# Optimization experiments

Hardware: AMD Instinct MI355X
Metric: run time of the kernel (lower is better)

## Reference

```python
import jax, jax.numpy as jnp
import numpy as np

N = 8192   # num_nodes
H = 128    # hidden_dim
B = 100    # batch of events
K = 5      # num_neg_samples
TD_MAX = 10000.0
TIME_SD = jnp.array([50.0, 7.0, 15.0, 15.0])  # time_sd from forward; time_mean = 0


def setup_inputs() -> dict:
    key = jax.random.key(0)
    ks = jax.random.split(key, 16)
    p = 32.0 / N  # avg degree ~32
    A = (jax.random.uniform(ks[0], (N, N)) < p).astype(jnp.float32)
    # S init: S[v,u] = 1/D[v] for neighbors u (row-normalized A)
    S = A / (A.sum(axis=1, keepdims=True) + 1e-7)
    z0 = jax.random.normal(ks[1], (N, H)) * 0.1
    u = jax.random.randint(ks[2], (B,), 0, N)
    v = jax.random.randint(ks[3], (B,), 0, N)
    event_types = jax.random.randint(ks[4], (B,), 0, 2)
    neg_idx = jax.random.randint(ks[5], (B, 2 * K), 0, N)
    time_diff = jax.random.normal(ks[6], (B, 2, 4))
    t_bar = jax.random.uniform(ks[7], (B, N)) * 1000.0
    t = 1000.0 + 10.0 * jnp.arange(B, dtype=jnp.float32)

    def lin(k, o, i):
        k1, k2 = jax.random.split(k)
        lim = 1.0 / np.sqrt(i)
        return (jax.random.uniform(k1, (o, i), minval=-lim, maxval=lim),
                jax.random.uniform(k2, (o,), minval=-lim, maxval=lim))

    om0_w, om0_b = lin(ks[8], 1, 2 * H)
    om1_w, om1_b = lin(ks[9], 1, 2 * H)
    Wh_w, Wh_b = lin(ks[10], H, H)
    Ws_w, Ws_b = lin(ks[11], H, H)
    Wr_w, Wr_b = lin(ks[12], H, H)
    Wt_w, Wt_b = lin(ks[13], H, 4)
    return dict(u=u, v=v, event_types=event_types, neg_idx=neg_idx,
                time_diff=time_diff, t_bar=t_bar, t=t, z0=z0, A=A, S=S,
                w_t=0.5 * jnp.ones(2), alpha=0.5 * jnp.ones(2), psi=0.5 * jnp.ones(2),
                om0_w=om0_w, om0_b=om0_b, om1_w=om1_w, om1_b=om1_b,
                Wh_w=Wh_w, Wh_b=Wh_b, Ws_w=Ws_w, Ws_b=Ws_b,
                Wr_w=Wr_w, Wr_b=Wr_b, Wt_w=Wt_w, Wt_b=Wt_b)


def _forward(u, v, event_types, neg_idx, time_diff, t_bar, t, z0, A, S,
             w_t, alpha, psi, om0_w, om0_b, om1_w, om1_b,
             Wh_w, Wh_b, Ws_w, Ws_b, Wr_w, Wr_b, Wt_w, Wt_b):
    td_norm = time_diff / TIME_SD  # (td - 0) / sd

    def hawkes(zu, zv, et, td):
        # lambda = psi * log(1 + exp(g/psi)) + alpha * exp(-w_t * td/td_max)
        zc = jnp.concatenate([zu, zv], axis=-1)
        g0 = jnp.einsum('...d,d->...', zc, om0_w[0]) + om0_b[0]
        g1 = jnp.einsum('...d,d->...', zc, om1_w[0]) + om1_b[0]
        g = jnp.where(et == 0, g0, g1)
        ps, al, wt = psi[et], alpha[et], w_t[et]
        gp = jnp.clip(g / (ps + 1e-7), -75.0, 75.0)
        return ps * jnp.log1p(jnp.exp(gp)) + al * jnp.exp(-wt * (td / TD_MAX))

    ar = jnp.arange(N)

    def step(z, ev):
        u_it, v_it, et, td2, tb, t_it, neg = ev
        z_u, z_v = z[u_it], z[v_it]
        Wh_all = z @ Wh_w.T + Wh_b  # [N,H]

        def struct(node):
            # structural attention over node's neighbors (masked, not dense loop)
            mask = A[node] > 0
            q = jnp.exp(S[node]) * mask
            q = q / (q.sum() + 1e-7)
            hsig = jax.nn.sigmoid(q[:, None] * Wh_all)
            hmax = jnp.where(mask[:, None], hsig, -jnp.inf).max(axis=0)
            return jnp.where(jnp.any(mask), hmax, 0.0)

        # update of u uses struct info from v's neighborhood, and vice versa
        hs = jnp.stack([struct(v_it), struct(u_it)])  # [2,H]
        h = (hs @ Ws_w.T + Ws_b) + (jnp.stack([z_u, z_v]) @ Wr_w.T + Wr_b) + (td2 @ Wt_w.T + Wt_b)
        z_upd = jax.nn.sigmoid(h)
        z_new = z.at[u_it].set(z_upd[0]).at[v_it].set(z_upd[1])

        # negative pairs: (u, v_neg_k) then (u_neg_k, v), using z_prev
        v_neg, u_neg = neg[:K], neg[K:]
        zu_neg = jnp.concatenate([jnp.broadcast_to(z_u, (K, H)), z[u_neg]], 0)
        zv_neg = jnp.concatenate([z[v_neg], jnp.broadcast_to(z_v, (K, H))], 0)
        lt_u = jnp.concatenate([jnp.full((K,), tb[u_it]), tb[u_neg]])
        lt_v = jnp.concatenate([tb[v_neg], jnp.full((K,), tb[v_it])])
        ts_neg = t_it - jnp.maximum(lt_u, lt_v)
        ts_pos = t_it - jnp.maximum(tb[u_it], tb[v_it])

        # all-node intensity prediction (Lambda_dict path, detached in torch)
        zd = jax.lax.stop_gradient(z)
        zu_all = jnp.concatenate([jnp.broadcast_to(jax.lax.stop_gradient(z_u), (N, H)),
                                  jnp.broadcast_to(jax.lax.stop_gradient(z_v), (N, H))], 0)
        zv_all = jnp.concatenate([zd, zd], 0)
        last_t = jnp.maximum(
            jnp.concatenate([jnp.full((N,), tb[u_it]), jnp.full((N,), tb[v_it])]),
            jnp.concatenate([tb, tb]))
        lam_all = hawkes(zu_all, zv_all, jnp.full((2 * N,), et),
                         jax.lax.stop_gradient(t_it - last_t))
        m = ((ar != u_it) & (ar != v_it)).astype(lam_all.dtype)
        lam_sum = jax.lax.stop_gradient(jnp.sum(lam_all * jnp.concatenate([m, m])))

        return z_new, (z_u, z_v, zu_neg, zv_neg, ts_pos, ts_neg, lam_sum)

    _, (zu_p, zv_p, zun, zvn, ts_p, ts_n, lam_sums) = jax.lax.scan(
        step, z0, (u, v, event_types, td_norm, t_bar, t, neg_idx))

    lam_pos = hawkes(zu_p, zv_p, event_types, ts_p)            # [B]
    lam_neg = hawkes(zun, zvn, event_types[:, None], ts_n)      # [B,2K]
    return jnp.concatenate([lam_pos[:, None], lam_neg, lam_sums[:, None]], axis=1)  # [B, 2K+2]


def reference(u, v, event_types, neg_idx, time_diff, t_bar, t, z0, A, S,
              w_t, alpha, psi, om0_w, om0_b, om1_w, om1_b,
              Wh_w, Wh_b, Ws_w, Ws_b, Wr_w, Wr_b, Wt_w, Wt_b):
    return _forward(u, v, event_types, neg_idx, time_diff, t_bar, t, z0, A, S,
                    w_t, alpha, psi, om0_w, om0_b, om1_w, om1_b,
                    Wh_w, Wh_b, Ws_w, Ws_b, Wr_w, Wr_b, Wt_w, Wt_b)
```

## Files before the change

### kernel.cpp

```cpp
#include <hip/hip_runtime.h>
#include <math.h>

#define N 8192
#define H 128
#define BB 100
#define KK 5
#define MAXN 256
#define TD_MAXF 10000.0f

#define OFF_WHALLV ((size_t)N * H)
#define OFF_ZVER (OFF_WHALLV + 2 * BB * H)
#define WH_LDW 132

#define AGENT_LD(p) \
  __hip_atomic_load((p), __ATOMIC_RELAXED, __HIP_MEMORY_SCOPE_AGENT)
#define AGENT_ST(p, v) \
  __hip_atomic_store((p), (v), __ATOMIC_RELAXED, __HIP_MEMORY_SCOPE_AGENT)

__global__ __launch_bounds__(256) void prep2_kernel(
    const float* __restrict__ z0, const float* __restrict__ om0,
    const float* __restrict__ om1, float* __restrict__ dvec0,
    unsigned* __restrict__ done) {
  if (blockIdx.x == 32) {
    if (threadIdx.x < 4) AGENT_ST(&done[threadIdx.x], 0u);
    return;
  }
  int j = blockIdx.x * 256 + threadIdx.x;
  const float4* zr = (const float4*)(z0 + (size_t)j * H);
  const float4* o0 = (const float4*)om0;
  const float4* o1 = (const float4*)om1;
  float a0 = 0, b0 = 0, a1 = 0, b1 = 0;
  for (int k = 0; k < H / 4; ++k) {
    float4 zv = zr[k];
    float4 l0 = o0[k], r0 = o0[k + H / 4];
    float4 l1 = o1[k], r1 = o1[k + H / 4];
    a0 += zv.x * l0.x + zv.y * l0.y + zv.z * l0.z + zv.w * l0.w;
    b0 += zv.x * r0.x + zv.y * r0.y + zv.z * r0.z + zv.w * r0.w;
    a1 += zv.x * l1.x + zv.y * l1.y + zv.z * l1.z + zv.w * l1.w;
    b1 += zv.x * r1.x + zv.y * r1.y + zv.z * r1.z + zv.w * r1.w;
  }
  dvec0[0 * N + j] = a0;
  dvec0[1 * N + j] = b0;
  dvec0[2 * N + j] = a1;
  dvec0[3 * N + j] = b1;
}

__global__ __launch_bounds__(1024, 4) void fused_kernel(
    const int* __restrict__ u_, const int* __restrict__ v_,
    const int* __restrict__ et_, const int* __restrict__ neg_,
    const float* __restrict__ time_diff, const float* __restrict__ t_bar,
    const float* __restrict__ tt, const float* __restrict__ z0,
    const float* __restrict__ A, const float* __restrict__ S,
    const float* __restrict__ Wh, const float* __restrict__ Ws,
    const float* __restrict__ Wr, const float* __restrict__ Wh_b,
    const float* __restrict__ Ws_b, const float* __restrict__ Wr_b,
    const float* __restrict__ Wt_w, const float* __restrict__ Wt_b,
    const float* __restrict__ w_t, const float* __restrict__ alpha,
    const float* __restrict__ psi, const float* __restrict__ om0_w,
    const float* __restrict__ om1_w, const float* __restrict__ om0_b,
    const float* __restrict__ om1_b, const float* __restrict__ wsf,
    float* __restrict__ zver, float* __restrict__ whallv,
    float* __restrict__ dlog, const float* __restrict__ dvec0,
    unsigned* done, float* __restrict__ out) {
  const int blk = blockIdx.x;
  const int t = threadIdx.x;
  __shared__ __align__(16) float WhL[H * WH_LDW];
  __shared__ float scratch[8][2][H];
  __shared__ float hsS[2][H];
  __shared__ float zrowS[2][H];
  __shared__ float zupdS[2][H];
  __shared__ float td2S[2][4];
  __shared__ int nidxS[2][MAXN];
  __shared__ float nqS[2][MAXN];
  __shared__ int woffS[2][MAXN];
  __shared__ int cMS[2];
  __shared__ int zsrcS[2];
  __shared__ unsigned needS[4];
  __shared__ int uL[BB], vL[BB];
  __shared__ int wsumI[16];
  __shared__ float wsumF[16];
  __shared__ float dR[N];
  __shared__ float red[1024];
  __shared__ float suS, svS;

  if (blk < BB) {
    const int b = blk;
    const int r = t >> 9;
    const int tr = t & 511;
    const int sub = (t >> 7) & 3;
    const int d = t & (H - 1);
    const int ks = t >> 7;
    const int k0 = ks * 16;

    if (t < BB) {
      uL[t] = u_[t];
      vL[t] = v_[t];
    }
    if (t >= 512 && t < 520) {
      int i = t - 512;
      int cc = i & 3;
      float sd = (cc == 0) ? 50.0f : ((cc == 1) ? 7.0f : 15.0f);
      td2S[i >> 2][cc] = time_diff[b * 8 + i] / sd;
    }
    if (t >= 1020) needS[t - 1020] = 0u;
    {
      const float4* wh4 = (const float4*)Wh;
      float4* whl4 = (float4*)WhL;
      for (int i = t; i < H * H / 4; i += 1024)
        whl4[(i >> 5) * 33 + (i & 31)] = wh4[i];
    }
    const float whb = Wh_b[d];
    float wsReg[16], wrReg[16], whReg[16];
#pragma unroll
    for (int kk = 0; kk < 16; ++kk) {
      wsReg[kk] = Ws[(size_t)d * H + k0 + kk];
      wrReg[kk] = Wr[(size_t)d * H + k0 + kk];
      whReg[kk] = Wh[(size_t)d * H + k0 + kk];
    }
    float biasReg = 0.0f;
    float4 wt4Reg = {0.0f, 0.0f, 0.0f, 0.0f};
    if (t < 256) {
      int dd = t & (H - 1);
      biasReg = Ws_b[dd] + Wr_b[dd] + Wt_b[dd];
      wt4Reg = ((const float4*)Wt_w)[dd];
    }
    float omA = 0.0f, omB = 0.0f;
    if (t >= 256 && t < 768) {
      int w = (t - 256) >> 6;
      int lane6 = t & 63;
      int which = w & 3;
      int wsel = which >> 1;
      int offo = (which & 1) * H;
      const float* omw = wsel ? om1_w : om0_w;
      omA = omw[offo + lane6];
      omB = omw[offo + 64 + lane6];
    }

    const int node = r ? u_[b] : v_[b];
    unsigned hm = 0u;
    int c = 0;
    float local = 0.0f;
    for (int it = 0; it < N / 512; ++it) {
      int j = it * 512 + tr;
      if (A[(size_t)node * N + j] > 0.0f) {
        hm |= 1u << it;
        ++c;
        local += expf(S[(size_t)node * N + j]);
      }
    }
    const int lane = t & 63;
    const int wv = t >> 6;
    int ex = c;
    for (int s2 = 1; s2 < 64; s2 <<= 1) {
      int o = __shfl_up(ex, s2);
      if (lane >= s2) ex += o;
    }
    float ls = local;
    for (int s2 = 32; s2 > 0; s2 >>= 1) ls += __shfl_down(ls, s2);
    if (lane == 63) wsumI[wv] = ex;
    if (lane == 0) wsumF[wv] = ls;
    ex -= c;
    __syncthreads();

    int base0 = 0, ctot = 0;
    float qs = 0.0f;
    {
      int w0 = r * 8;
#pragma unroll
      for (int w = 0; w < 8; ++w) {
        int wi = w0 + w;
        int cw = wsumI[wi];
        if (wi < wv) base0 += cw;
        ctot += cw;
        qs += wsumF[wi];
      }
    }
    const float iq = 1.0f / (qs + 1e-7f);
    int p = base0 + ex;
    for (int it = 0; it < N / 512; ++it) {
      if ((hm >> it) & 1u) {
        int j = it * 512 + tr;
        if (p < MAXN) {
          nidxS[r][p] = j;
          nqS[r][p] = expf(S[(size_t)node * N + j]);
        }
        ++p;
      }
    }
    const int cM = min(ctot, MAXN);
    if (tr == 0) cMS[r] = cM;
    __syncthreads();

    for (int i = tr; i < cM; i += 512) {
      int n = nidxS[r][i];
      int a = -1, row = 0;
      for (int s2 = b - 1; s2 >= 0; --s2) {
        if (vL[s2] == n) { a = s2; row = 1; break; }
        if (uL[s2] == n) { a = s2; row = 0; break; }
      }
      woffS[r][i] = (a < 0) ? n * H : (int)OFF_WHALLV + (2 * a + row) * H;
      nqS[r][i] *= iq;
      if (a >= 0) atomicOr(&needS[a >> 5], 1u << (a & 31));
    }
    if (t < 2) {
      int nd = t ? vL[b] : uL[b];
      int a = -1, row = 0;
      for (int s2 = b - 1; s2 >= 0; --s2) {
        if (vL[s2] == nd) { a = s2; row = 1; break; }
        if (uL[s2] == nd) { a = s2; row = 0; break; }
      }
      zsrcS[t] = (a >= 0) ? 2 * a + row : -1;
      if (a >= 0) atomicOr(&needS[a >> 5], 1u << (a & 31));
    }
    __syncthreads();

    float zpre = 0.0f;
    int zs = -1;
    if (t < 256) {
      int rr = t >> 7, dd = t & (H - 1);
      zs = zsrcS[rr];
      if (zs < 0) {
        int nd = rr ? vL[b] : uL[b];
        zpre = z0[(size_t)nd * H + dd];
      }
    }

    float mx = -INFINITY;
    {
      const float4* WhL4 = (const float4*)WhL;
      for (int i = sub; i < cM; i += 4) {
        int off = woffS[r][i];
        if (off < (int)OFF_WHALLV) {
          const float4* zr4 = (const float4*)(z0 + (size_t)(off >> 7) * H);
          float acc = whb;
#pragma unroll 8
          for (int m = 0; m < 32; ++m) {
            float4 zv = zr4[m];
            float4 wvv = WhL4[d * 33 + m];
            acc += zv.x * wvv.x + zv.y * wvv.y + zv.z * wvv.z + zv.w * wvv.w;
          }
          mx = fmaxf(mx, nqS[r][i] * acc);
        }
      }
    }
    if (t == 0) {
      for (int w = 0; w < 4; ++w) {
        unsigned nw = needS[w];
        if (!nw) continue;
        while ((AGENT_LD(&done[w]) & nw) != nw) __builtin_amdgcn_s_sleep(1);
      }
    }
    __syncthreads();

    const int ub = uL[b], vb = vL[b];

    for (int i = sub; i < cM; i += 4) {
      int off = woffS[r][i];
      if (off >= (int)OFF_WHALLV)
        mx = fmaxf(mx, nqS[r][i] * AGENT_LD(&wsf[(size_t)off + d]));
    }
    scratch[sub][r][d] = mx;
    if (t < 256) {
      int rr = t >> 7, dd = t & (H - 1);
      zrowS[rr][dd] =
          (zs < 0) ? zpre : AGENT_LD(&wsf[OFF_ZVER + (size_t)zs * H + dd]);
    }
    __syncthreads();

    if (t < 2 * H) {
      int rr = t >> 7, dd = t & (H - 1);
      float m = fmaxf(fmaxf(scratch[0][rr][dd], scratch[1][rr][dd]),
                      fmaxf(scratch[2][rr][dd], scratch[3][rr][dd]));
      hsS[rr][dd] = (cMS[rr] > 0) ? (1.0f / (1.0f + expf(-m))) : 0.0f;
    }
    __syncthreads();

    {
      float a0 = 0.0f, a1 = 0.0f;
#pragma unroll
      for (int kk = 0; kk < 16; ++kk) {
        int k = k0 + kk;
        a0 += hsS[0][k] * wsReg[kk] + zrowS[0][k] * wrReg[kk];
        a1 += hsS[1][k] * wsReg[kk] + zrowS[1][k] * wrReg[kk];
      }
      scratch[ks][0][d] = a0;
      scratch[ks][1][d] = a1;
    }
    __syncthreads();

    if (t < 2 * H) {
      int rr = t >> 7, dd = t & (H - 1);
      float acc = biasReg;
#pragma unroll
      for (int kx = 0; kx < 8; ++kx) acc += scratch[kx][rr][dd];
      acc += td2S[rr][0] * wt4Reg.x + td2S[rr][1] * wt4Reg.y +
             td2S[rr][2] * wt4Reg.z + td2S[rr][3] * wt4Reg.w;
      float zu = 1.0f / (1.0f + expf(-acc));
      zupdS[rr][dd] = zu;
      AGENT_ST(&zver[(size_t)(2 * b + rr) * H + dd], zu);
    }
    __syncthreads();

    {
      int r0 = (ub == vb) ? 1 : 0;
      float f0 = 0.0f, f1 = 0.0f;
#pragma unroll
      for (int kk = 0; kk < 16; ++kk) {
        int k = k0 + kk;
        f0 += zupdS[r0][k] * whReg[kk];
        f1 += zupdS[1][k] * whReg[kk];
      }
      scratch[ks][0][d] = f0;
      scratch[ks][1][d] = f1;
    }
    __syncthreads();

    if (t < 2 * H) {
      int rr = t >> 7, dd = t & (H - 1);
      float acc = whb;
#pragma unroll
      for (int kx = 0; kx < 8; ++kx) acc += scratch[kx][rr][dd];
      AGENT_ST(&whallv[(size_t)(2 * b + rr) * H + dd], acc);
    } else if (t < 768) {
      int w = (t - 256) >> 6;
      int lane6 = t & 63;
      int row = w >> 2;
      int which = w & 3;
      int rr = (row == 0 && ub == vb) ? 1 : row;
      float val = zupdS[rr][lane6] * omA + zupdS[rr][64 + lane6] * omB;
      for (int s2 = 32; s2 > 0; s2 >>= 1) val += __shfl_down(val, s2);
      if (lane6 == 0) AGENT_ST(&dlog[b * 8 + which * 2 + row], val);
    }
    __syncthreads();

    if (t == 0) {
      asm volatile("s_waitcnt vmcnt(0)" ::: "memory");
      __hip_atomic_fetch_or(&done[b >> 5], 1u << (b & 31), __ATOMIC_RELAXED,
                            __HIP_MEMORY_SCOPE_AGENT);
    }
    return;
  }

  const int b = blk - BB;
  const int e = et_[b];
  const int ub = u_[b], vb = v_[b];
  const float ps = psi[e], al = alpha[e], wt = w_t[e];
  const float ob0 = om0_b[0], ob1 = om1_b[0];
  const float ob = e ? ob1 : ob0;
  const float tcur = tt[b];
  const float inv_ps = 1.0f / (ps + 1e-7f);
  const int whichR = 2 * e + 1;
  const int whichL = 2 * e;

  if (t < BB) {
    uL[t] = u_[t];
    vL[t] = v_[t];
  }
  {
    const float4* base = (const float4*)(dvec0 + (size_t)whichR * N);
    float4* dst = (float4*)dR;
    for (int i = t; i < N / 4; i += 1024) dst[i] = base[i];
  }
  if (t == 0) {
    for (int w = 0; w < 4; ++w) {
      int cb = b - 32 * w;
      unsigned nw =
          (cb >= 32) ? 0xffffffffu : (cb <= 0 ? 0u : ((1u << cb) - 1u));
      if (!nw) continue;
      while ((AGENT_LD(&done[w]) & nw) != nw) __builtin_amdgcn_s_sleep(1);
    }
  }
  __syncthreads();

  for (int i = t; i < b; i += 1024) {
    int ui = uL[i], vi = vL[i];
    bool u_over = (ui == vi);
    bool v_over = false;
    for (int j = i + 1; j < b; ++j) {
      int uj = uL[j], vj = vL[j];
      u_over = u_over || (uj == ui) || (vj == ui);
      v_over = v_over || (uj == vi) || (vj == vi);
    }
    if (!u_over) dR[ui] = AGENT_LD(&dlog[i * 8 + whichR * 2 + 0]);
    if (!v_over) dR[vi] = AGENT_LD(&dlog[i * 8 + whichR * 2 + 1]);
  }

  if (t < 13) {
    auto dpre = [&](int x, int which) -> float {
      for (int bp = b - 1; bp >= 0; --bp) {
        if (vL[bp] == x) return AGENT_LD(&dlog[bp * 8 + which * 2 + 1]);
        if (uL[bp] == x) return AGENT_LD(&dlog[bp * 8 + which * 2 + 0]);
      }
      return dvec0[(size_t)which * N + x];
    };
    if (t < 11) {
      int li, ri;
      float ltu, ltv;
      if (t == 0) {
        li = ub; ri = vb;
        ltu = t_bar[(size_t)b * N + ub];
        ltv = t_bar[(size_t)b * N + vb];
      } else if (t <= 5) {
        int vn = neg_[b * (2 * KK) + (t - 1)];
        li = ub; ri = vn;
        ltu = t_bar[(size_t)b * N + ub];
        ltv = t_bar[(size_t)b * N + vn];
      } else {
        int un = neg_[b * (2 * KK) + (t - 1)];
        li = un; ri = vb;
        ltu = t_bar[(size_t)b * N + un];
        ltv = t_bar[(size_t)b * N + vb];
      }
      float g = dpre(li, whichL) + dpre(ri, whichR) + ob;
      float gp = fminf(fmaxf(g * inv_ps, -75.0f), 75.0f);
      float ts = tcur - fmaxf(ltu, ltv);
      out[b * 12 + t] = ps * log1pf(expf(gp)) + al * expf(-wt * (ts / TD_MAXF));
    } else if (t == 11) {
      suS = dpre(ub, whichL);
    } else {
      svS = dpre(vb, whichL);
    }
  }
  __syncthreads();

  const float su = suS, sv = svS;
  const float tb_u = t_bar[(size_t)b * N + ub];
  const float tb_v = t_bar[(size_t)b * N + vb];
  const float Ku = expf((su + ob) * inv_ps);
  const float Kv = expf((sv + ob) * inv_ps);
  const float Cx = al * expf(-wt * (tcur / TD_MAXF));
  const float Eu = expf(wt * (tb_u / TD_MAXF));
  const float Ev = expf(wt * (tb_v / TD_MAXF));
  const float wTD = wt / TD_MAXF;
  const float4* tb4 = (const float4*)(t_bar + (size_t)b * N);
  const float4* dR4 = (const float4*)dR;
  float acc = 0.0f;
  for (int j4 = t; j4 < N / 4; j4 += 1024) {
    float4 dv = dR4[j4];
    float4 tb = tb4[j4];
    float de[4] = {dv.x, dv.y, dv.z, dv.w};
    float te[4] = {tb.x, tb.y, tb.z, tb.w};
#pragma unroll
    for (int ee = 0; ee < 4; ++ee) {
      int j = j4 * 4 + ee;
      if (j == ub || j == vb) continue;
      float Dj = expf(de[ee] * inv_ps);
      float spl = ps * (log1pf(Ku * Dj) + log1pf(Kv * Dj));
      float Ej = expf(wTD * te[ee]);
      float ex2 = Cx * (fmaxf(Eu, Ej) + fmaxf(Ev, Ej));
      acc += spl + ex2;
    }
  }
  red[t] = acc;
  __syncthreads();
  for (int s2 = 512; s2 > 0; s2 >>= 1) {
    if (t < s2) red[t] += red[t + s2];
    __syncthreads();
  }
  if (t == 0) out[b * 12 + 11] = red[0];
}

extern "C" void kernel_launch(void* const* d_in, const int* in_sizes, int n_in,
                              void* d_out, int out_size, void* d_ws,
                              size_t ws_size, hipStream_t stream) {
  const int* u = (const int*)d_in[0];
  const int* v = (const int*)d_in[1];
  const int* et = (const int*)d_in[2];
  const int* neg = (const int*)d_in[3];
  const float* time_diff = (const float*)d_in[4];
  const float* t_bar = (const float*)d_in[5];
  const float* t = (const float*)d_in[6];
  const float* z0 = (const float*)d_in[7];
  const float* A = (const float*)d_in[8];
  const float* S = (const float*)d_in[9];
  const float* w_t = (const float*)d_in[10];
  const float* alpha = (const float*)d_in[11];
  const float* psi = (const float*)d_in[12];
  const float* om0_w = (const float*)d_in[13];
  const float* om0_b = (const float*)d_in[14];
  const float* om1_w = (const float*)d_in[15];
  const float* om1_b = (const float*)d_in[16];
  const float* Wh_w = (const float*)d_in[17];
  const float* Wh_b = (const float*)d_in[18];
  const float* Ws_w = (const float*)d_in[19];
  const float* Ws_b = (const float*)d_in[20];
  const float* Wr_w = (const float*)d_in[21];
  const float* Wr_b = (const float*)d_in[22];
  const float* Wt_w = (const float*)d_in[23];
  const float* Wt_b = (const float*)d_in[24];
  float* out = (float*)d_out;

  float* wsf = (float*)d_ws;
  float* whallv = wsf + OFF_WHALLV;
  float* zver = wsf + OFF_ZVER;
  float* dvec0 = zver + 2 * BB * H;
  float* dlog = dvec0 + 4 * N;
  unsigned* done = (unsigned*)(dlog + 8 * BB);

  prep2_kernel<<<33, 256, 0, stream>>>(z0, om0_w, om1_w, dvec0, done);
  fused_kernel<<<2 * BB, 1024, 0, stream>>>(
      u, v, et, neg, time_diff, t_bar, t, z0, A, S, Wh_w, Ws_w, Wr_w, Wh_b,
      Ws_b, Wr_b, Wt_w, Wt_b, w_t, alpha, psi, om0_w, om1_w, om0_b, om1_b,
      wsf, zver, whallv, dlog, dvec0, done, out);
}
```

Before: 603.8 us.

## Precompute Wh·z0 for all nodes and transpose weight matrices in prep

Adds a prep kernel that transposes Wh, Ws and Wr into workspace, plus a new kernel that computes Wh·z0+b for all 8192 nodes up front. The fused kernel then reads the precomputed rows instead of doing a per-neighbor 128-long dot product against a shared-memory copy of Wh, and the 66KB WhL shared buffer is dropped. Register weight loads become coalesced over d. The trade-off is computing all N rows, including ones never used, and two extra launches, in exchange for less per-block compute, less LDS and possibly higher occupancy.

```diff
diff --git a/kernel.cpp b/kernel.cpp
--- a/kernel.cpp
+++ b/kernel.cpp
@@ -10,39 +10,70 @@
 
 #define OFF_WHALLV ((size_t)N * H)
 #define OFF_ZVER (OFF_WHALLV + 2 * BB * H)
-#define WH_LDW 132
 
 #define AGENT_LD(p) \
   __hip_atomic_load((p), __ATOMIC_RELAXED, __HIP_MEMORY_SCOPE_AGENT)
 #define AGENT_ST(p, v) \
   __hip_atomic_store((p), (v), __ATOMIC_RELAXED, __HIP_MEMORY_SCOPE_AGENT)
 
-__global__ __launch_bounds__(256) void prep2_kernel(
-    const float* __restrict__ z0, const float* __restrict__ om0,
-    const float* __restrict__ om1, float* __restrict__ dvec0,
-    unsigned* __restrict__ done) {
-  if (blockIdx.x == 32) {
-    if (threadIdx.x < 4) AGENT_ST(&done[threadIdx.x], 0u);
-    return;
-  }
-  int j = blockIdx.x * 256 + threadIdx.x;
-  const float4* zr = (const float4*)(z0 + (size_t)j * H);
-  const float4* o0 = (const float4*)om0;
-  const float4* o1 = (const float4*)om1;
-  float a0 = 0, b0 = 0, a1 = 0, b1 = 0;
-  for (int k = 0; k < H / 4; ++k) {
-    float4 zv = zr[k];
-    float4 l0 = o0[k], r0 = o0[k + H / 4];
-    float4 l1 = o1[k], r1 = o1[k + H / 4];
-    a0 += zv.x * l0.x + zv.y * l0.y + zv.z * l0.z + zv.w * l0.w;
-    b0 += zv.x * r0.x + zv.y * r0.y + zv.z * r0.z + zv.w * r0.w;
-    a1 += zv.x * l1.x + zv.y * l1.y + zv.z * l1.z + zv.w * l1.w;
-    b1 += zv.x * r1.x + zv.y * r1.y + zv.z * r1.z + zv.w * r1.w;
-  }
-  dvec0[0 * N + j] = a0;
-  dvec0[1 * N + j] = b0;
-  dvec0[2 * N + j] = a1;
-  dvec0[3 * N + j] = b1;
+__global__ __launch_bounds__(256) void prep_kernel(
+    const float* __restrict__ Wh, const float* __restrict__ Ws,
+    const float* __restrict__ Wr, const float* __restrict__ z0,
+    const float* __restrict__ om0, const float* __restrict__ om1,
+    float* __restrict__ WhT, float* __restrict__ WsT, float* __restrict__ WrT,
+    float* __restrict__ dvec0, unsigned* __restrict__ done) {
+  const int B0 = H * H, B1 = 2 * H * H, B2 = 3 * H * H;
+  const int B3 = B2 + 4;
+  int idx = blockIdx.x * 256 + threadIdx.x;
+  if (idx < B0) {
+    int d = idx >> 7, k = idx & (H - 1);
+    WhT[k * H + d] = Wh[d * H + k];
+  } else if (idx < B1) {
+    int e = idx - B0;
+    int d = e >> 7, k = e & (H - 1);
+    WsT[k * H + d] = Ws[d * H + k];
+  } else if (idx < B2) {
+    int e = idx - B1;
+    int d = e >> 7, k = e & (H - 1);
+    WrT[k * H + d] = Wr[d * H + k];
+  } else if (idx < B3) {
+    AGENT_ST(&done[idx - B2], 0u);
+  } else if (idx < B3 + N) {
+    int j = idx - B3;
+    const float4* zr = (const float4*)(z0 + (size_t)j * H);
+    const float4* o0 = (const float4*)om0;
+    const float4* o1 = (const float4*)om1;
+    float a0 = 0, b0 = 0, a1 = 0, b1 = 0;
+    for (int k = 0; k < H / 4; ++k) {
+      float4 zv = zr[k];
+      float4 l0 = o0[k], r0 = o0[k + H / 4];
+      float4 l1 = o1[k], r1 = o1[k + H / 4];
+      a0 += zv.x * l0.x + zv.y * l0.y + zv.z * l0.z + zv.w * l0.w;
+      b0 += zv.x * r0.x + zv.y * r0.y + zv.z * r0.z + zv.w * r0.w;
+      a1 += zv.x * l1.x + zv.y * l1.y + zv.z * l1.z + zv.w * l1.w;
+      b1 += zv.x * r1.x + zv.y * r1.y + zv.z * r1.z + zv.w * r1.w;
+    }
+    dvec0[0 * N + j] = a0;
+    dvec0[1 * N + j] = b0;
+    dvec0[2 * N + j] = a1;
+    dvec0[3 * N + j] = b1;
+  }
+}
+
+__global__ __launch_bounds__(256) void whall_kernel(
+    const float* __restrict__ z0, const float* __restrict__ WhT,
+    const float* __restrict__ Wh_b, float* __restrict__ whall) {
+  const int blk = blockIdx.x;
+  const int tid = threadIdx.x;
+  __shared__ float zr2[2][H];
+  int r = tid >> 7, d = tid & (H - 1);
+  int row = blk * 2 + r;
+  zr2[r][d] = z0[(size_t)row * H + d];
+  __syncthreads();
+  float acc = Wh_b[d];
+#pragma unroll 8
+  for (int k = 0; k < H; ++k) acc += zr2[r][k] * WhT[k * H + d];
+  whall[(size_t)row * H + d] = acc;
 }
 
 __global__ __launch_bounds__(1024, 4) void fused_kernel(
@@ -51,8 +82,8 @@
     const float* __restrict__ time_diff, const float* __restrict__ t_bar,
     const float* __restrict__ tt, const float* __restrict__ z0,
     const float* __restrict__ A, const float* __restrict__ S,
-    const float* __restrict__ Wh, const float* __restrict__ Ws,
-    const float* __restrict__ Wr, const float* __restrict__ Wh_b,
+    const float* __restrict__ WhT, const float* __restrict__ WsT,
+    const float* __restrict__ WrT, const float* __restrict__ Wh_b,
     const float* __restrict__ Ws_b, const float* __restrict__ Wr_b,
     const float* __restrict__ Wt_w, const float* __restrict__ Wt_b,
     const float* __restrict__ w_t, const float* __restrict__ alpha,
@@ -64,7 +95,6 @@
     unsigned* done, float* __restrict__ out) {
   const int blk = blockIdx.x;
   const int t = threadIdx.x;
-  __shared__ __align__(16) float WhL[H * WH_LDW];
   __shared__ float scratch[8][2][H];
   __shared__ float hsS[2][H];
   __shared__ float zrowS[2][H];
@@ -103,19 +133,13 @@
       td2S[i >> 2][cc] = time_diff[b * 8 + i] / sd;
     }
     if (t >= 1020) needS[t - 1020] = 0u;
-    {
-      const float4* wh4 = (const float4*)Wh;
-      float4* whl4 = (float4*)WhL;
-      for (int i = t; i < H * H / 4; i += 1024)
-        whl4[(i >> 5) * 33 + (i & 31)] = wh4[i];
-    }
     const float whb = Wh_b[d];
     float wsReg[16], wrReg[16], whReg[16];
 #pragma unroll
     for (int kk = 0; kk < 16; ++kk) {
-      wsReg[kk] = Ws[(size_t)d * H + k0 + kk];
-      wrReg[kk] = Wr[(size_t)d * H + k0 + kk];
-      whReg[kk] = Wh[(size_t)d * H + k0 + kk];
+      wsReg[kk] = WsT[(k0 + kk) * H + d];
+      wrReg[kk] = WrT[(k0 + kk) * H + d];
+      whReg[kk] = WhT[(k0 + kk) * H + d];
     }
     float biasReg = 0.0f;
     float4 wt4Reg = {0.0f, 0.0f, 0.0f, 0.0f};
@@ -226,22 +250,10 @@
     }
 
     float mx = -INFINITY;
-    {
-      const float4* WhL4 = (const float4*)WhL;
-      for (int i = sub; i < cM; i += 4) {
-        int off = woffS[r][i];
-        if (off < (int)OFF_WHALLV) {
-          const float4* zr4 = (const float4*)(z0 + (size_t)(off >> 7) * H);
-          float acc = whb;
-#pragma unroll 8
-          for (int m = 0; m < 32; ++m) {
-            float4 zv = zr4[m];
-            float4 wvv = WhL4[d * 33 + m];
-            acc += zv.x * wvv.x + zv.y * wvv.y + zv.z * wvv.z + zv.w * wvv.w;
-          }
-          mx = fmaxf(mx, nqS[r][i] * acc);
-        }
-      }
+    for (int i = sub; i < cM; i += 4) {
+      int off = woffS[r][i];
+      if (off < (int)OFF_WHALLV)
+        mx = fmaxf(mx, nqS[r][i] * wsf[(size_t)off + d]);
     }
     if (t == 0) {
       for (int w = 0; w < 4; ++w) {
@@ -491,15 +503,22 @@
   float* out = (float*)d_out;
 
   float* wsf = (float*)d_ws;
+  float* whall = wsf;
   float* whallv = wsf + OFF_WHALLV;
   float* zver = wsf + OFF_ZVER;
-  float* dvec0 = zver + 2 * BB * H;
+  float* WhT = zver + 2 * BB * H;
+  float* WsT = WhT + H * H;
+  float* WrT = WsT + H * H;
+  float* dvec0 = WrT + H * H;
   float* dlog = dvec0 + 4 * N;
   unsigned* done = (unsigned*)(dlog + 8 * BB);
 
-  prep2_kernel<<<33, 256, 0, stream>>>(z0, om0_w, om1_w, dvec0, done);
+  const int PREP_ELEMS = 3 * H * H + 4 + N;
+  prep_kernel<<<(PREP_ELEMS + 255) / 256, 256, 0, stream>>>(
+      Wh_w, Ws_w, Wr_w, z0, om0_w, om1_w, WhT, WsT, WrT, dvec0, done);
+  whall_kernel<<<N / 2, 256, 0, stream>>>(z0, WhT, Wh_b, whall);
   fused_kernel<<<2 * BB, 1024, 0, stream>>>(
-      u, v, et, neg, time_diff, t_bar, t, z0, A, S, Wh_w, Ws_w, Wr_w, Wh_b,
+      u, v, et, neg, time_diff, t_bar, t, z0, A, S, WhT, WsT, WrT, Wh_b,
       Ws_b, Wr_b, Wt_w, Wt_b, w_t, alpha, psi, om0_w, om1_w, om0_b, om1_b,
       wsf, zver, whallv, dlog, dvec0, done, out);
 }
```

Measured after the change: 583.7 us. -3.3%, faster.

## Precompute Wh·z0 for all nodes cooperatively inside fused kernel and drop prep kernel

Applied to the files above, without the earlier changes.

Each of the first 100 blocks now computes Wh·z0 for a chunk of 82 rows into a global table, signals through an atomic counter, and then reads neighbour projections from that table instead of recomputing per-neighbour matvecs from an LDS copy of Wh. The omega dot-products formerly done by a separate prep kernel are computed by the second group of blocks with a grid-wide counter barrier, and the counters are zeroed with a memset. The A row is also loaded into registers up front. This is meant to remove redundant matvecs and one kernel launch, at the cost of spin-wait barriers that depend on all blocks being co-resident, plus a full N×H table write.

```diff
diff --git a/kernel.cpp b/kernel.cpp
--- a/kernel.cpp
+++ b/kernel.cpp
@@ -7,43 +7,15 @@
 #define KK 5
 #define MAXN 256
 #define TD_MAXF 10000.0f
+#define CH 82
 
 #define OFF_WHALLV ((size_t)N * H)
 #define OFF_ZVER (OFF_WHALLV + 2 * BB * H)
-#define WH_LDW 132
 
 #define AGENT_LD(p) \
   __hip_atomic_load((p), __ATOMIC_RELAXED, __HIP_MEMORY_SCOPE_AGENT)
 #define AGENT_ST(p, v) \
   __hip_atomic_store((p), (v), __ATOMIC_RELAXED, __HIP_MEMORY_SCOPE_AGENT)
-
-__global__ __launch_bounds__(256) void prep2_kernel(
-    const float* __restrict__ z0, const float* __restrict__ om0,
-    const float* __restrict__ om1, float* __restrict__ dvec0,
-    unsigned* __restrict__ done) {
-  if (blockIdx.x == 32) {
-    if (threadIdx.x < 4) AGENT_ST(&done[threadIdx.x], 0u);
-    return;
-  }
-  int j = blockIdx.x * 256 + threadIdx.x;
-  const float4* zr = (const float4*)(z0 + (size_t)j * H);
-  const float4* o0 = (const float4*)om0;
-  const float4* o1 = (const float4*)om1;
-  float a0 = 0, b0 = 0, a1 = 0, b1 = 0;
-  for (int k = 0; k < H / 4; ++k) {
-    float4 zv = zr[k];
-    float4 l0 = o0[k], r0 = o0[k + H / 4];
-    float4 l1 = o1[k], r1 = o1[k + H / 4];
-    a0 += zv.x * l0.x + zv.y * l0.y + zv.z * l0.z + zv.w * l0.w;
-    b0 += zv.x * r0.x + zv.y * r0.y + zv.z * r0.z + zv.w * r0.w;
-    a1 += zv.x * l1.x + zv.y * l1.y + zv.z * l1.z + zv.w * l1.w;
-    b1 += zv.x * r1.x + zv.y * r1.y + zv.z * r1.z + zv.w * r1.w;
-  }
-  dvec0[0 * N + j] = a0;
-  dvec0[1 * N + j] = b0;
-  dvec0[2 * N + j] = a1;
-  dvec0[3 * N + j] = b1;
-}
 
 __global__ __launch_bounds__(1024, 4) void fused_kernel(
     const int* __restrict__ u_, const int* __restrict__ v_,
@@ -59,12 +31,12 @@
     const float* __restrict__ psi, const float* __restrict__ om0_w,
     const float* __restrict__ om1_w, const float* __restrict__ om0_b,
     const float* __restrict__ om1_b, const float* __restrict__ wsf,
-    float* __restrict__ zver, float* __restrict__ whallv,
-    float* __restrict__ dlog, const float* __restrict__ dvec0,
-    unsigned* done, float* __restrict__ out) {
+    float* __restrict__ whall, float* __restrict__ zver,
+    float* __restrict__ whallv, float* __restrict__ dlog,
+    float* __restrict__ dvec0, unsigned* done, unsigned* cnts,
+    float* __restrict__ out) {
   const int blk = blockIdx.x;
   const int t = threadIdx.x;
-  __shared__ __align__(16) float WhL[H * WH_LDW];
   __shared__ float scratch[8][2][H];
   __shared__ float hsS[2][H];
   __shared__ float zrowS[2][H];
@@ -103,13 +75,38 @@
       td2S[i >> 2][cc] = time_diff[b * 8 + i] / sd;
     }
     if (t >= 1020) needS[t - 1020] = 0u;
+    const float whb = Wh_b[d];
+
     {
-      const float4* wh4 = (const float4*)Wh;
-      float4* whl4 = (float4*)WhL;
-      for (int i = t; i < H * H / 4; i += 1024)
-        whl4[(i >> 5) * 33 + (i & 31)] = wh4[i];
-    }
-    const float whb = Wh_b[d];
+      const int rowbase = b * CH;
+      const int rcnt = min(CH, N - rowbase);
+      const int slot = t >> 7;
+      const float4* wh4 = (const float4*)(Wh + (size_t)d * H);
+      for (int it2 = 0; it2 < (CH + 7) / 8; ++it2) {
+        int ridx = it2 * 8 + slot;
+        int row = rowbase + ridx;
+        bool ok = ridx < rcnt;
+        if (ok) scratch[slot][0][d] = z0[(size_t)row * H + d];
+        __syncthreads();
+        if (ok) {
+          const float* zr = &scratch[slot][0][0];
+          float acc = whb;
+#pragma unroll 8
+          for (int m = 0; m < 32; ++m) {
+            float4 w4 = wh4[m];
+            acc += zr[4 * m] * w4.x + zr[4 * m + 1] * w4.y +
+                   zr[4 * m + 2] * w4.z + zr[4 * m + 3] * w4.w;
+          }
+          AGENT_ST(&whall[(size_t)row * H + d], acc);
+        }
+        __syncthreads();
+      }
+      if (t == 0) {
+        __hip_atomic_fetch_add(&cnts[0], 1u, __ATOMIC_RELAXED,
+                               __HIP_MEMORY_SCOPE_AGENT);
+      }
+    }
+
     float wsReg[16], wrReg[16], whReg[16];
 #pragma unroll
     for (int kk = 0; kk < 16; ++kk) {
@@ -137,15 +134,19 @@
     }
 
     const int node = r ? u_[b] : v_[b];
+    float aReg[16];
+#pragma unroll
+    for (int it = 0; it < 16; ++it)
+      aReg[it] = A[(size_t)node * N + it * 512 + tr];
     unsigned hm = 0u;
     int c = 0;
     float local = 0.0f;
-    for (int it = 0; it < N / 512; ++it) {
-      int j = it * 512 + tr;
-      if (A[(size_t)node * N + j] > 0.0f) {
+#pragma unroll
+    for (int it = 0; it < 16; ++it) {
+      if (aReg[it] > 0.0f) {
         hm |= 1u << it;
         ++c;
-        local += expf(S[(size_t)node * N + j]);
+        local += expf(S[(size_t)node * N + it * 512 + tr]);
       }
     }
     const int lane = t & 63;
@@ -177,7 +178,7 @@
     }
     const float iq = 1.0f / (qs + 1e-7f);
     int p = base0 + ex;
-    for (int it = 0; it < N / 512; ++it) {
+    for (int it = 0; it < 16; ++it) {
       if ((hm >> it) & 1u) {
         int j = it * 512 + tr;
         if (p < MAXN) {
@@ -225,23 +226,15 @@
       }
     }
 
+    if (t == 0) {
+      while (AGENT_LD(&cnts[0]) < (unsigned)BB) __builtin_amdgcn_s_sleep(1);
+    }
+    __syncthreads();
     float mx = -INFINITY;
-    {
-      const float4* WhL4 = (const float4*)WhL;
-      for (int i = sub; i < cM; i += 4) {
-        int off = woffS[r][i];
-        if (off < (int)OFF_WHALLV) {
-          const float4* zr4 = (const float4*)(z0 + (size_t)(off >> 7) * H);
-          float acc = whb;
-#pragma unroll 8
-          for (int m = 0; m < 32; ++m) {
-            float4 zv = zr4[m];
-            float4 wvv = WhL4[d * 33 + m];
-            acc += zv.x * wvv.x + zv.y * wvv.y + zv.z * wvv.z + zv.w * wvv.w;
-          }
-          mx = fmaxf(mx, nqS[r][i] * acc);
-        }
-      }
+    for (int i = sub; i < cM; i += 4) {
+      int off = woffS[r][i];
+      if (off < (int)OFF_WHALLV)
+        mx = fmaxf(mx, nqS[r][i] * AGENT_LD(&wsf[(size_t)off + d]));
     }
     if (t == 0) {
       for (int w = 0; w < 4; ++w) {
@@ -357,10 +350,37 @@
     vL[t] = v_[t];
   }
   {
-    const float4* base = (const float4*)(dvec0 + (size_t)whichR * N);
-    float4* dst = (float4*)dR;
-    for (int i = t; i < N / 4; i += 1024) dst[i] = base[i];
-  }
+    const int rowbase = b * CH;
+    const int rcnt = min(CH, N - rowbase);
+    if (t < rcnt) {
+      int j = rowbase + t;
+      const float4* zr = (const float4*)(z0 + (size_t)j * H);
+      const float4* o0 = (const float4*)om0_w;
+      const float4* o1 = (const float4*)om1_w;
+      float a0 = 0, b0 = 0, a1 = 0, b1 = 0;
+      for (int k = 0; k < H / 4; ++k) {
+        float4 zv = zr[k];
+        float4 l0 = o0[k], r0 = o0[k + H / 4];
+        float4 l1 = o1[k], r1 = o1[k + H / 4];
+        a0 += zv.x * l0.x + zv.y * l0.y + zv.z * l0.z + zv.w * l0.w;
+        b0 += zv.x * r0.x + zv.y * r0.y + zv.z * r0.z + zv.w * r0.w;
+        a1 += zv.x * l1.x + zv.y * l1.y + zv.z * l1.z + zv.w * l1.w;
+        b1 += zv.x * r1.x + zv.y * r1.y + zv.z * r1.z + zv.w * r1.w;
+      }
+      AGENT_ST(&dvec0[0 * N + j], a0);
+      AGENT_ST(&dvec0[1 * N + j], b0);
+      AGENT_ST(&dvec0[2 * N + j], a1);
+      AGENT_ST(&dvec0[3 * N + j], b1);
+    }
+    __syncthreads();
+    if (t == 0) {
+      __hip_atomic_fetch_add(&cnts[1], 1u, __ATOMIC_RELAXED,
+                             __HIP_MEMORY_SCOPE_AGENT);
+      while (AGENT_LD(&cnts[1]) < (unsigned)BB) __builtin_amdgcn_s_sleep(1);
+    }
+    __syncthreads();
+  }
+  for (int i = t; i < N; i += 1024) dR[i] = AGENT_LD(&dvec0[whichR * N + i]);
   if (t == 0) {
     for (int w = 0; w < 4; ++w) {
       int cb = b - 32 * w;
@@ -391,7 +411,7 @@
         if (vL[bp] == x) return AGENT_LD(&dlog[bp * 8 + which * 2 + 1]);
         if (uL[bp] == x) return AGENT_LD(&dlog[bp * 8 + which * 2 + 0]);
       }
-      return dvec0[(size_t)which * N + x];
+      return AGENT_LD(&dvec0[(size_t)which * N + x]);
     };
     if (t < 11) {
       int li, ri;
@@ -491,15 +511,17 @@
   float* out = (float*)d_out;
 
   float* wsf = (float*)d_ws;
+  float* whall = wsf;
   float* whallv = wsf + OFF_WHALLV;
   float* zver = wsf + OFF_ZVER;
   float* dvec0 = zver + 2 * BB * H;
   float* dlog = dvec0 + 4 * N;
   unsigned* done = (unsigned*)(dlog + 8 * BB);
-
-  prep2_kernel<<<33, 256, 0, stream>>>(z0, om0_w, om1_w, dvec0, done);
+  unsigned* cnts = done + 4;
+
+  hipMemsetAsync(done, 0, 6 * sizeof(unsigned), stream);
   fused_kernel<<<2 * BB, 1024, 0, stream>>>(
       u, v, et, neg, time_diff, t_bar, t, z0, A, S, Wh_w, Ws_w, Wr_w, Wh_b,
       Ws_b, Wr_b, Wt_w, Wt_b, w_t, alpha, psi, om0_w, om1_w, om0_b, om1_b,
-      wsf, zver, whallv, dlog, dvec0, done, out);
+      wsf, whall, zver, whallv, dlog, dvec0, done, cnts, out);
 }
```

Result: slower. 707.8 us (+17.2%).
